# Performance work log

Measured on AMD Instinct MI355X. Metric: run time of the kernel, lower is better.

Reference implementation:

```python
import jax, jax.numpy as jnp
import numpy as np

# Hair-bundle model parameters (params list)
LAM, LAM_A = 1.0, 10.0          # drag coefficients of bundle / adaptation motor
K_GS, K_SP = 0.75, 0.6          # gating-spring and pivot stiffness
D0, DELTA = 0.5, 0.2            # gating swing and gating sensitivity
F_MAX, S_CA = 1.0, 0.7          # max motor force, Ca feedback strength
C_M, TAU_M = 1.5, 1.0           # motor Ca binding rate / time constant
C_GS, TAU_GS = 1.2, 5.0         # gating-spring Ca binding rate / time constant
C_T, TAU_T = 0.8, 10.0          # transduction Ca binding rate / time constant
HB_NOISE, A_NOISE = 0.05, 0.02  # diffusion amplitudes (constant, used by g)
# force_params
AMP, OMEGA = 0.3, 6.283185307179586

N_SAMPLES = 8_388_608  # ensemble of SDE sample paths
STATE_DIM = 5          # [X, Xa, pm, pgs, pt]


def setup_inputs() -> dict:
    key = jax.random.key(0)
    k_t, k_x = jax.random.split(key)
    t = jax.random.uniform(k_t, (1,), dtype=jnp.float32)
    x = 0.1 * jax.random.normal(k_x, (N_SAMPLES, STATE_DIM), dtype=jnp.float32)
    return {"t": t, "x": x}


def reference(t, x):
    # Fully vectorized drift f(t, x) over the sample axis (replaces the
    # per-sample Python loop + sympy lambda eval in the torch module).
    X, Xa, pm, pgs, pt = x[:, 0], x[:, 1], x[:, 2], x[:, 3], x[:, 4]
    p_open = jax.nn.sigmoid((X - Xa - D0) / DELTA)     # channel open prob
    f_gs = K_GS * (X - Xa - D0 * p_open)               # gating-spring force
    force = AMP * jnp.sin(OMEGA * t[0])                # sin_driving_force(t)
    dX = (-f_gs - K_SP * X) / LAM + force              # force added to var 0 only
    dXa = (f_gs - F_MAX * (1.0 - S_CA * pm)) / LAM_A
    dpm = (C_M * p_open * (1.0 - pm) - pm) / TAU_M
    dpgs = (C_GS * p_open * (1.0 - pgs) - pgs) / TAU_GS
    dpt = (C_T * p_open * (1.0 - pt) - pt) / TAU_T
    return jnp.stack([dX, dXa, dpm, dpgs, dpt], axis=-1)  # [N, 5]
```

## Files before the change

kernel.cpp:

```cpp
#include <hip/hip_runtime.h>


namespace {

typedef float f32x4 __attribute__((ext_vector_type(4)));

constexpr float K_GS      = 0.75f;
constexpr float K_SP      = 0.6f;
constexpr float D0        = 0.5f;
constexpr float DELTA_INV = 5.0f;
constexpr float F_MAX     = 1.0f;
constexpr float S_CA      = 0.7f;
constexpr float LAMA_INV  = 0.1f;
constexpr float AMP       = 0.3f;
constexpr float OMEGA     = 6.283185307179586f;

constexpr int BLOCK       = 256;
constexpr int ROWS_PER_T  = 4;
constexpr int CHUNK_ROWS  = BLOCK * ROWS_PER_T;
constexpr int CHUNK_F4    = CHUNK_ROWS * 5 / 4;
constexpr int WAVE_F4     = 64 * ROWS_PER_T * 5 / 4;

__device__ __forceinline__ void compute_row(float X, float Xa, float pm, float pgs, float pt,
                                            float force, float* o) {
    float d   = X - Xa;
    float z   = (d - D0) * DELTA_INV;
    float p   = 1.0f / (1.0f + __expf(-z));
    float fgs = K_GS * (d - D0 * p);
    o[0] = force - fgs - K_SP * X;
    o[1] = (fgs - (F_MAX - S_CA * pm)) * LAMA_INV;
    o[2] = 1.5f * p * (1.0f - pm) - pm;
    o[3] = (1.2f * p * (1.0f - pgs) - pgs) * 0.2f;
    o[4] = (0.8f * p * (1.0f - pt)  - pt)  * 0.1f;
}

}

__global__ __launch_bounds__(BLOCK) void hb_kernel(
        const float* __restrict__ tp,
        const float* __restrict__ xp,
        float* __restrict__ op,
        long long nrows) {
    __shared__ f32x4 s[CHUNK_F4];

    const int tid   = threadIdx.x;
    const int lane  = tid & 63;
    const int wbase = (tid >> 6) * WAVE_F4;

    const long long chunk0 = (long long)blockIdx.x * CHUNK_ROWS;

    const float force = AMP * sinf(OMEGA * tp[0]);

    if (chunk0 + CHUNK_ROWS <= nrows) {
        const f32x4* gsrc = reinterpret_cast<const f32x4*>(xp + chunk0 * 5) + wbase;
        f32x4*       gdst = reinterpret_cast<f32x4*>(op + chunk0 * 5)       + wbase;
        f32x4*       sw   = s + wbase;

#pragma unroll
        for (int k = 0; k < 5; ++k)
            sw[64 * k + lane] = __builtin_nontemporal_load(gsrc + 64 * k + lane);

        __builtin_amdgcn_wave_barrier();

        f32x4* r4 = reinterpret_cast<f32x4*>(reinterpret_cast<float*>(sw) + lane * 20);

        float vals[20];
#pragma unroll
        for (int k = 0; k < 5; ++k) {
            f32x4 v = r4[k];
            vals[4*k+0] = v.x; vals[4*k+1] = v.y; vals[4*k+2] = v.z; vals[4*k+3] = v.w;
        }

#pragma unroll
        for (int r = 0; r < ROWS_PER_T; ++r)
            compute_row(vals[5*r+0], vals[5*r+1], vals[5*r+2], vals[5*r+3], vals[5*r+4],
                        force, &vals[5*r]);

#pragma unroll
        for (int k = 0; k < 5; ++k)
            r4[k] = (f32x4){vals[4*k+0], vals[4*k+1], vals[4*k+2], vals[4*k+3]};

        __builtin_amdgcn_wave_barrier();

#pragma unroll
        for (int k = 0; k < 5; ++k)
            __builtin_nontemporal_store(sw[64 * k + lane], gdst + 64 * k + lane);
    } else {
        for (long long r = chunk0 + tid * ROWS_PER_T;
             r < nrows && r < chunk0 + (long long)(tid + 1) * ROWS_PER_T; ++r) {
            float in[5], out[5];
            for (int j = 0; j < 5; ++j) in[j] = xp[r*5 + j];
            compute_row(in[0], in[1], in[2], in[3], in[4], force, out);
            for (int j = 0; j < 5; ++j) op[r*5 + j] = out[j];
        }
    }
}

extern "C" void kernel_launch(void* const* d_in, const int* in_sizes, int n_in,
                              void* d_out, int out_size, void* d_ws, size_t ws_size,
                              hipStream_t stream) {
    const float* t = (const float*)d_in[0];
    const float* x = (const float*)d_in[1];
    float* out     = (float*)d_out;

    const long long nrows = (long long)in_sizes[1] / 5;
    const int grid = (int)((nrows + CHUNK_ROWS - 1) / CHUNK_ROWS);

    hb_kernel<<<grid, BLOCK, 0, stream>>>(t, x, out, nrows);
}
```

Measured before the change: 270.4 us.

## Process four chunks per block with register-prefetched next-chunk loads

Each block now walks CPB=4 consecutive chunks instead of one. The next chunk's global loads are issued into registers before the current chunk is computed and stored, so memory latency overlaps with compute and stores. This cuts the grid size by four and amortizes block launch and the sinf setup. The cost is fewer resident waves to hide latency, plus higher register pressure from holding the prefetched data.

```diff
diff --git a/kernel.cpp b/kernel.cpp
--- a/kernel.cpp
+++ b/kernel.cpp
@@ -20,6 +20,7 @@
 constexpr int CHUNK_ROWS  = BLOCK * ROWS_PER_T;
 constexpr int CHUNK_F4    = CHUNK_ROWS * 5 / 4;
 constexpr int WAVE_F4     = 64 * ROWS_PER_T * 5 / 4;
+constexpr int CPB         = 4;
 
 __device__ __forceinline__ void compute_row(float X, float Xa, float pm, float pgs, float pt,
                                             float force, float* o) {
@@ -47,47 +48,67 @@
     const int lane  = tid & 63;
     const int wbase = (tid >> 6) * WAVE_F4;
 
-    const long long chunk0 = (long long)blockIdx.x * CHUNK_ROWS;
+    f32x4* sw = s + wbase;
+    f32x4* r4 = reinterpret_cast<f32x4*>(reinterpret_cast<float*>(sw) + lane * 20);
 
     const float force = AMP * sinf(OMEGA * tp[0]);
 
-    if (chunk0 + CHUNK_ROWS <= nrows) {
-        const f32x4* gsrc = reinterpret_cast<const f32x4*>(xp + chunk0 * 5) + wbase;
-        f32x4*       gdst = reinterpret_cast<f32x4*>(op + chunk0 * 5)       + wbase;
-        f32x4*       sw   = s + wbase;
+    const long long nchunks = (nrows + CHUNK_ROWS - 1) / CHUNK_ROWS;
+    const long long nfull   = nrows / CHUNK_ROWS;
+    const long long cstart  = (long long)blockIdx.x * CPB;
+    long long cend = cstart + CPB; if (cend > nchunks) cend = nchunks;
+    long long cfe  = cend < nfull ? cend : nfull;
+
+    long long c = cstart;
+    if (c < cfe) {
+        f32x4 rin[5];
+        {
+            const f32x4* g = reinterpret_cast<const f32x4*>(xp + c * (long long)CHUNK_ROWS * 5)
+                             + wbase + lane;
+#pragma unroll
+            for (int k = 0; k < 5; ++k) rin[k] = __builtin_nontemporal_load(g + 64 * k);
+        }
+
+        for (; c < cfe; ++c) {
+#pragma unroll
+            for (int k = 0; k < 5; ++k) sw[64 * k + lane] = rin[k];
+            __builtin_amdgcn_wave_barrier();
+
+            float vals[20];
+#pragma unroll
+            for (int k = 0; k < 5; ++k) {
+                f32x4 v = r4[k];
+                vals[4*k+0] = v.x; vals[4*k+1] = v.y; vals[4*k+2] = v.z; vals[4*k+3] = v.w;
+            }
+
+            if (c + 1 < cfe) {
+                const f32x4* g = reinterpret_cast<const f32x4*>(
+                                     xp + (c + 1) * (long long)CHUNK_ROWS * 5) + wbase + lane;
+#pragma unroll
+                for (int k = 0; k < 5; ++k) rin[k] = __builtin_nontemporal_load(g + 64 * k);
+            }
 
 #pragma unroll
-        for (int k = 0; k < 5; ++k)
-            sw[64 * k + lane] = __builtin_nontemporal_load(gsrc + 64 * k + lane);
-
-        __builtin_amdgcn_wave_barrier();
-
-        f32x4* r4 = reinterpret_cast<f32x4*>(reinterpret_cast<float*>(sw) + lane * 20);
-
-        float vals[20];
-#pragma unroll
-        for (int k = 0; k < 5; ++k) {
-            f32x4 v = r4[k];
-            vals[4*k+0] = v.x; vals[4*k+1] = v.y; vals[4*k+2] = v.z; vals[4*k+3] = v.w;
-        }
+            for (int r = 0; r < ROWS_PER_T; ++r)
+                compute_row(vals[5*r+0], vals[5*r+1], vals[5*r+2], vals[5*r+3], vals[5*r+4],
+                            force, &vals[5*r]);
 
 #pragma unroll
-        for (int r = 0; r < ROWS_PER_T; ++r)
-            compute_row(vals[5*r+0], vals[5*r+1], vals[5*r+2], vals[5*r+3], vals[5*r+4],
-                        force, &vals[5*r]);
+            for (int k = 0; k < 5; ++k)
+                r4[k] = (f32x4){vals[4*k+0], vals[4*k+1], vals[4*k+2], vals[4*k+3]};
+            __builtin_amdgcn_wave_barrier();
 
+            f32x4* gd = reinterpret_cast<f32x4*>(op + c * (long long)CHUNK_ROWS * 5)
+                        + wbase + lane;
 #pragma unroll
-        for (int k = 0; k < 5; ++k)
-            r4[k] = (f32x4){vals[4*k+0], vals[4*k+1], vals[4*k+2], vals[4*k+3]};
+            for (int k = 0; k < 5; ++k)
+                __builtin_nontemporal_store(sw[64 * k + lane], gd + 64 * k);
+            __builtin_amdgcn_wave_barrier();
+        }
+    }
 
-        __builtin_amdgcn_wave_barrier();
-
-#pragma unroll
-        for (int k = 0; k < 5; ++k)
-            __builtin_nontemporal_store(sw[64 * k + lane], gdst + 64 * k + lane);
-    } else {
-        for (long long r = chunk0 + tid * ROWS_PER_T;
-             r < nrows && r < chunk0 + (long long)(tid + 1) * ROWS_PER_T; ++r) {
+    if (nfull < cend && nfull >= cstart) {
+        for (long long r = nfull * (long long)CHUNK_ROWS + tid; r < nrows; r += BLOCK) {
             float in[5], out[5];
             for (int j = 0; j < 5; ++j) in[j] = xp[r*5 + j];
             compute_row(in[0], in[1], in[2], in[3], in[4], force, out);
@@ -103,8 +124,9 @@
     const float* x = (const float*)d_in[1];
     float* out     = (float*)d_out;
 
-    const long long nrows = (long long)in_sizes[1] / 5;
-    const int grid = (int)((nrows + CHUNK_ROWS - 1) / CHUNK_ROWS);
+    const long long nrows   = (long long)in_sizes[1] / 5;
+    const long long nchunks = (nrows + CHUNK_ROWS - 1) / CHUNK_ROWS;
+    const int grid = (int)((nchunks + CPB - 1) / CPB);
 
     hb_kernel<<<grid, BLOCK, 0, stream>>>(t, x, out, nrows);
 }
```

After: 277.0 us. +2.4%, slower.
